# Performance work log

Hardware: AMD Instinct MI355X
Metric: run time of the kernel (lower is better)

The kernel has to match this reference:

```python
import jax, jax.numpy as jnp
import numpy as np

B, H, I, E, K = 512, 1024, 1024, 32, 4
EPS, ALPHA, LIMIT = 1e-5, 1.702, 7.0


def _swiglu(h):
    # interleaved split: even cols -> glu path, odd cols -> linear path
    x_glu = jnp.minimum(h[..., ::2], LIMIT)
    x_lin = jnp.clip(h[..., 1::2], -LIMIT, LIMIT)
    return x_glu * jax.nn.sigmoid(ALPHA * x_glu) * (x_lin + 1.0)


def setup_inputs() -> dict:
    key = jax.random.key(0)
    ks = jax.random.split(key, 7)
    n = lambda k, shape, s: jax.random.normal(k, shape, dtype=jnp.float32) * s
    return {
        "x": n(ks[0], (B, H), 1.0),
        "norm_scale": jnp.ones((H,), jnp.float32),
        "gate_w": n(ks[1], (E, H), 0.02),
        "gate_b": n(ks[2], (E,), 0.02),
        "mlp1_w": n(ks[3], (E, 2 * I, H), 0.02),
        "mlp1_b": n(ks[4], (E, 2 * I), 0.02),
        "mlp2_w": n(ks[5], (E, H, I), 0.02),
        "mlp2_b": n(ks[6], (E, H), 0.02),
    }


def reference(x, norm_scale, gate_w, gate_b, mlp1_w, mlp1_b, mlp2_w, mlp2_b):
    # RMSNorm in fp32
    t = x * jax.lax.rsqrt(jnp.mean(x * x, axis=-1, keepdims=True) + EPS) * norm_scale
    # gate + top-k routing; softmax over the k selected logits
    g = t @ gate_w.T + gate_b                      # [B, E]
    vals, idx = jax.lax.top_k(g, K)                # [B, K]
    w = jax.nn.softmax(vals, axis=-1)              # [B, K]
    # dense routing weights [B, E]: w_dense[b, e] = sum_k w[b,k] * (idx[b,k]==e)
    w_dense = jnp.zeros((t.shape[0], gate_w.shape[0]), t.dtype)
    w_dense = w_dense.at[jnp.arange(t.shape[0])[:, None], idx].add(w)
    # grouped-dense equivalent of the per-token gathered einsum:
    # original: einsum('beck,bk->bec', mlp1_w[idx], t); here we compute all
    # experts densely and combine with w_dense (zero for unselected experts),
    # which is the same math without materializing [B,K,2I,H] weights.
    h = jnp.einsum('bk,eck->bec', t, mlp1_w) + mlp1_b   # [B, E, 2I]
    a = _swiglu(h)                                       # [B, E, I]
    o = jnp.einsum('bei,ehi->beh', a, mlp2_w) + mlp2_b   # [B, E, H]
    y = jnp.einsum('beh,be->bh', o, w_dense)             # [B, H]
    return x + y
```

## Files before the change

### kernel.cpp

```cpp
#include <hip/hip_runtime.h>
#include <hip/hip_bf16.h>
#include <math.h>


#define NB   512
#define NH   1024
#define NI   1024
#define NE   32
#define NK   4
#define N2I  2048
#define CAP  512
#define PADK 40

static constexpr float EPS   = 1e-5f;
static constexpr float ALPHA = 1.702f;
static constexpr float LIMIT = 7.0f;

typedef short bf16x8 __attribute__((ext_vector_type(8)));
typedef float f32x4  __attribute__((ext_vector_type(4)));

__device__ __forceinline__ short hi16(float x) {
    return (short)(__float_as_uint(x) >> 16);
}
__device__ __forceinline__ short lo16(float x) {
    unsigned hb = __float_as_uint(x) & 0xFFFF0000u;
    float r = x - __uint_as_float(hb);
    return (short)(__float_as_uint(r) >> 16);
}
__device__ __forceinline__ void cvt8r(float4 v0, float4 v1,
                                      bf16x8& hh, bf16x8& ll) {
    float f[8] = {v0.x, v0.y, v0.z, v0.w, v1.x, v1.y, v1.z, v1.w};
#pragma unroll
    for (int i = 0; i < 8; i++) { hh[i] = hi16(f[i]); ll[i] = lo16(f[i]); }
}

__global__ __launch_bounds__(256) void k_rms_gate(
    const float* __restrict__ x, const float* __restrict__ scale,
    const float* __restrict__ gw, const float* __restrict__ gb,
    float* __restrict__ t, int* __restrict__ cnt,
    int* __restrict__ tok, int* __restrict__ tke, float* __restrict__ tkw) {
    __shared__ float sh_t[NH];
    __shared__ float sh_red[4];
    __shared__ float sh_g[NE];
    const int b = blockIdx.x, tid = threadIdx.x;
    const int lane = tid & 63, wid = tid >> 6;

    float4 xv = reinterpret_cast<const float4*>(x + (size_t)b * NH)[tid];
    float ss = xv.x * xv.x + xv.y * xv.y + xv.z * xv.z + xv.w * xv.w;
#pragma unroll
    for (int o = 32; o >= 1; o >>= 1) ss += __shfl_down(ss, o);
    if (lane == 0) sh_red[wid] = ss;
    __syncthreads();
    const float tot = sh_red[0] + sh_red[1] + sh_red[2] + sh_red[3];
    const float r = rsqrtf(tot * (1.0f / NH) + EPS);
    float4 sv = reinterpret_cast<const float4*>(scale)[tid];
    float4 tv;
    tv.x = xv.x * r * sv.x; tv.y = xv.y * r * sv.y;
    tv.z = xv.z * r * sv.z; tv.w = xv.w * r * sv.w;
    reinterpret_cast<float4*>(sh_t)[tid] = tv;
    reinterpret_cast<float4*>(t + (size_t)b * NH)[tid] = tv;
    __syncthreads();

#pragma unroll
    for (int q = 0; q < 8; q++) {
        const int e = wid * 8 + q;
        const float* __restrict__ w = gw + (size_t)e * NH;
        float p = 0.f;
#pragma unroll
        for (int i = 0; i < 16; i++) { int k = lane + 64 * i; p += sh_t[k] * w[k]; }
#pragma unroll
        for (int o = 32; o >= 1; o >>= 1) p += __shfl_down(p, o);
        if (lane == 0) sh_g[e] = p + gb[e];
    }
    __syncthreads();

    if (tid == 0) {
        float gv[NE];
#pragma unroll
        for (int e = 0; e < NE; e++) gv[e] = sh_g[e];
        float vals[NK]; int ids[NK];
#pragma unroll
        for (int k = 0; k < NK; k++) {
            int bi = 0; float bv = gv[0];
            for (int e = 1; e < NE; e++) if (gv[e] > bv) { bv = gv[e]; bi = e; }
            vals[k] = bv; ids[k] = bi; gv[bi] = -1e30f;
        }
        const float m = vals[0];
        float s = 0.f, wv[NK];
#pragma unroll
        for (int k = 0; k < NK; k++) { wv[k] = __expf(vals[k] - m); s += wv[k]; }
        const float inv = 1.f / s;
#pragma unroll
        for (int k = 0; k < NK; k++) {
            const int e = ids[k];
            const int pos = atomicAdd(&cnt[e], 1);
            tok[e * CAP + pos] = b;
            tke[b * NK + k] = (e << 16) | pos;
            tkw[b * NK + k] = wv[k] * inv;
        }
    }
}

__global__ void k_prefix(const int* __restrict__ cnt, int* __restrict__ base) {
    if (threadIdx.x == 0) {
        int r = 0;
        for (int e = 0; e < NE; e++) { base[e] = r; r += cnt[e]; }
    }
}

__global__ __launch_bounds__(512, 2) void k_mlp1(
    const float* __restrict__ t, const float* __restrict__ w1,
    const float* __restrict__ b1, const int* __restrict__ cnt,
    const int* __restrict__ base, const int* __restrict__ tok,
    float* __restrict__ a) {
    const int e  = blockIdx.z;
    const int ne = cnt[e];
    const int m0 = blockIdx.y * 128;
    if (m0 >= ne) return;
    const int c0 = blockIdx.x * 128;
    const float* __restrict__ W = w1 + (size_t)e * N2I * NH + (size_t)c0 * NH;

    __shared__ short Ah[128][PADK], Al[128][PADK];
    __shared__ short Bh[128][PADK], Bl[128][PADK];
    __shared__ int   toks[128];

    const int tid = threadIdx.x;
    if (tid < 128) toks[tid] = (m0 + tid < ne) ? tok[e * CAP + m0 + tid] : -1;
    __syncthreads();

    const int lane = tid & 63;
    const int wid  = tid >> 6;
    const int wr = wid >> 1, wc = wid & 1;
    const int frow = lane & 15;
    const int fk   = (lane >> 4) * 8;
    const int srow = tid >> 2;
    const int sc8  = (tid & 3) * 8;

    f32x4 acc[2][4] = {};

    const int tka = toks[srow];
    const float* __restrict__ asrc = t + (size_t)(tka < 0 ? 0 : tka) * NH + sc8;
    const float* __restrict__ bsrc = W + (size_t)srow * NH + sc8;

    float4 ra0 = *(const float4*)(asrc);
    float4 ra1 = *(const float4*)(asrc + 4);
    float4 rb0 = *(const float4*)(bsrc);
    float4 rb1 = *(const float4*)(bsrc + 4);

    for (int k0 = 0; k0 < NH; k0 += 32) {
        bf16x8 hh, ll;
        cvt8r(ra0, ra1, hh, ll);
        if (tka < 0) { hh = (bf16x8)(short)0; ll = (bf16x8)(short)0; }
        *(bf16x8*)&Ah[srow][sc8] = hh;
        *(bf16x8*)&Al[srow][sc8] = ll;
        cvt8r(rb0, rb1, hh, ll);
        *(bf16x8*)&Bh[srow][sc8] = hh;
        *(bf16x8*)&Bl[srow][sc8] = ll;
        if (k0 + 32 < NH) {
            ra0 = *(const float4*)(asrc + k0 + 32);
            ra1 = *(const float4*)(asrc + k0 + 36);
            rb0 = *(const float4*)(bsrc + k0 + 32);
            rb1 = *(const float4*)(bsrc + k0 + 36);
        }
        __syncthreads();

        bf16x8 ah[2], al[2], bh[4], bl[4];
#pragma unroll
        for (int m = 0; m < 2; m++) {
            const int r = wr * 32 + m * 16 + frow;
            ah[m] = *(const bf16x8*)&Ah[r][fk];
            al[m] = *(const bf16x8*)&Al[r][fk];
        }
#pragma unroll
        for (int n = 0; n < 4; n++) {
            const int c = wc * 64 + n * 16 + frow;
            bh[n] = *(const bf16x8*)&Bh[c][fk];
            bl[n] = *(const bf16x8*)&Bl[c][fk];
        }
#pragma unroll
        for (int m = 0; m < 2; m++)
#pragma unroll
            for (int n = 0; n < 4; n++) {
                acc[m][n] = __builtin_amdgcn_mfma_f32_16x16x32_bf16(ah[m], bh[n], acc[m][n], 0, 0, 0);
                acc[m][n] = __builtin_amdgcn_mfma_f32_16x16x32_bf16(ah[m], bl[n], acc[m][n], 0, 0, 0);
                acc[m][n] = __builtin_amdgcn_mfma_f32_16x16x32_bf16(al[m], bh[n], acc[m][n], 0, 0, 0);
            }
        __syncthreads();
    }

    const int slot0 = base[e];
#pragma unroll
    for (int m = 0; m < 2; m++)
#pragma unroll
        for (int n = 0; n < 4; n++) {
            const int gcol = c0 + wc * 64 + n * 16 + frow;
            const float bias = b1[e * N2I + gcol];
            f32x4 v = acc[m][n];
#pragma unroll
            for (int j = 0; j < 4; j++) {
                const float h  = v[j] + bias;
                const float hp = __shfl_xor(h, 1);
                const int row = m0 + wr * 32 + m * 16 + (lane >> 4) * 4 + j;
                if (!(lane & 1) && row < ne) {
                    const float xg = fminf(h, LIMIT);
                    const float xl = fminf(fmaxf(hp, -LIMIT), LIMIT);
                    const float sg2 = 1.f / (1.f + __expf(-ALPHA * xg));
                    a[(size_t)(slot0 + row) * NI + (gcol >> 1)] = xg * sg2 * (xl + 1.f);
                }
            }
        }
}

__global__ __launch_bounds__(512, 2) void k_mlp2(
    const float* __restrict__ a, const float* __restrict__ w2,
    const float* __restrict__ b2, const int* __restrict__ cnt,
    const int* __restrict__ base, float* __restrict__ o) {
    const int e  = blockIdx.z;
    const int ne = cnt[e];
    const int m0 = blockIdx.y * 128;
    if (m0 >= ne) return;
    const int c0 = blockIdx.x * 128;
    const int slot0 = base[e];
    const float* __restrict__ W = w2 + (size_t)e * NH * NI + (size_t)c0 * NI;

    __shared__ short Ah[128][PADK], Al[128][PADK];
    __shared__ short Bh[128][PADK], Bl[128][PADK];

    const int tid = threadIdx.x;
    const int lane = tid & 63;
    const int wid  = tid >> 6;
    const int wr = wid >> 1, wc = wid & 1;
    const int frow = lane & 15;
    const int fk   = (lane >> 4) * 8;
    const int srow = tid >> 2;
    const int sc8  = (tid & 3) * 8;

    f32x4 acc[2][4] = {};

    const int mval = (m0 + srow < ne);
    const float* __restrict__ asrc =
        a + (size_t)(mval ? (slot0 + m0 + srow) : 0) * NI + sc8;
    const float* __restrict__ bsrc = W + (size_t)srow * NI + sc8;

    float4 ra0 = *(const float4*)(asrc);
    float4 ra1 = *(const float4*)(asrc + 4);
    float4 rb0 = *(const float4*)(bsrc);
    float4 rb1 = *(const float4*)(bsrc + 4);

    for (int k0 = 0; k0 < NI; k0 += 32) {
        bf16x8 hh, ll;
        cvt8r(ra0, ra1, hh, ll);
        if (!mval) { hh = (bf16x8)(short)0; ll = (bf16x8)(short)0; }
        *(bf16x8*)&Ah[srow][sc8] = hh;
        *(bf16x8*)&Al[srow][sc8] = ll;
        cvt8r(rb0, rb1, hh, ll);
        *(bf16x8*)&Bh[srow][sc8] = hh;
        *(bf16x8*)&Bl[srow][sc8] = ll;
        if (k0 + 32 < NI) {
            ra0 = *(const float4*)(asrc + k0 + 32);
            ra1 = *(const float4*)(asrc + k0 + 36);
            rb0 = *(const float4*)(bsrc + k0 + 32);
            rb1 = *(const float4*)(bsrc + k0 + 36);
        }
        __syncthreads();

        bf16x8 ah[2], al[2], bh[4], bl[4];
#pragma unroll
        for (int m = 0; m < 2; m++) {
            const int r = wr * 32 + m * 16 + frow;
            ah[m] = *(const bf16x8*)&Ah[r][fk];
            al[m] = *(const bf16x8*)&Al[r][fk];
        }
#pragma unroll
        for (int n = 0; n < 4; n++) {
            const int c = wc * 64 + n * 16 + frow;
            bh[n] = *(const bf16x8*)&Bh[c][fk];
            bl[n] = *(const bf16x8*)&Bl[c][fk];
        }
#pragma unroll
        for (int m = 0; m < 2; m++)
#pragma unroll
            for (int n = 0; n < 4; n++) {
                acc[m][n] = __builtin_amdgcn_mfma_f32_16x16x32_bf16(ah[m], bh[n], acc[m][n], 0, 0, 0);
                acc[m][n] = __builtin_amdgcn_mfma_f32_16x16x32_bf16(ah[m], bl[n], acc[m][n], 0, 0, 0);
                acc[m][n] = __builtin_amdgcn_mfma_f32_16x16x32_bf16(al[m], bh[n], acc[m][n], 0, 0, 0);
            }
        __syncthreads();
    }

#pragma unroll
    for (int m = 0; m < 2; m++)
#pragma unroll
        for (int n = 0; n < 4; n++) {
            const int gcol = c0 + wc * 64 + n * 16 + frow;
            const float bias = b2[e * NH + gcol];
            f32x4 v = acc[m][n];
#pragma unroll
            for (int j = 0; j < 4; j++) {
                const int row = m0 + wr * 32 + m * 16 + (lane >> 4) * 4 + j;
                if (row < ne)
                    o[(size_t)(slot0 + row) * NH + gcol] = v[j] + bias;
            }
        }
}

__global__ __launch_bounds__(256) void k_combine(
    const float* __restrict__ x, const float* __restrict__ o,
    const int* __restrict__ base, const int* __restrict__ tke,
    const float* __restrict__ tkw, float* __restrict__ out) {
    const int b = blockIdx.x, tid = threadIdx.x;
    int slots[NK]; float wk[NK];
#pragma unroll
    for (int k = 0; k < NK; k++) {
        const int v = tke[b * NK + k];
        slots[k] = base[v >> 16] + (v & 0xFFFF);
        wk[k] = tkw[b * NK + k];
    }
    float4 r = reinterpret_cast<const float4*>(x + (size_t)b * NH)[tid];
#pragma unroll
    for (int k = 0; k < NK; k++) {
        float4 ov = reinterpret_cast<const float4*>(o + (size_t)slots[k] * NH)[tid];
        r.x += wk[k] * ov.x; r.y += wk[k] * ov.y;
        r.z += wk[k] * ov.z; r.w += wk[k] * ov.w;
    }
    reinterpret_cast<float4*>(out + (size_t)b * NH)[tid] = r;
}

extern "C" void kernel_launch(void* const* d_in, const int* in_sizes, int n_in,
                              void* d_out, int out_size, void* d_ws, size_t ws_size,
                              hipStream_t stream) {
    const float* x     = (const float*)d_in[0];
    const float* scale = (const float*)d_in[1];
    const float* gw    = (const float*)d_in[2];
    const float* gb    = (const float*)d_in[3];
    const float* w1    = (const float*)d_in[4];
    const float* b1    = (const float*)d_in[5];
    const float* w2    = (const float*)d_in[6];
    const float* b2    = (const float*)d_in[7];
    float* out = (float*)d_out;

    float* t   = (float*)d_ws;
    float* a   = t + (size_t)NB * NH;
    float* o   = a + (size_t)NB * NK * NI;
    int*   tok = (int*)(o + (size_t)NB * NK * NH);
    int*   tke = tok + NE * CAP;
    float* tkw = (float*)(tke + NB * NK);
    int*   cnt = (int*)(tkw + NB * NK);
    int*   bse = cnt + NE;

    hipMemsetAsync(cnt, 0, NE * sizeof(int), stream);
    k_rms_gate<<<NB, 256, 0, stream>>>(x, scale, gw, gb, t, cnt, tok, tke, tkw);
    k_prefix<<<1, 64, 0, stream>>>(cnt, bse);
    k_mlp1<<<dim3(N2I / 128, NB / 128, NE), 512, 0, stream>>>(t, w1, b1, cnt, bse, tok, a);
    k_mlp2<<<dim3(NH / 128, NB / 128, NE), 512, 0, stream>>>(a, w2, b2, cnt, bse, o);
    k_combine<<<NB, 256, 0, stream>>>(x, o, bse, tke, tkw, out);
}
```

Before: 598.6 us.

## Drop weight low-part split, use 4 waves with larger per-wave tiles and double-buffered loads

Weights are now rounded to a single bf16 (round-to-nearest-even) rather than split into hi/lo parts. That removes one of the three MFMAs per tile and the Bl shared buffer, leaving activations as the only operand kept in split precision. Both MLP kernels move from 512 to 256 threads, so each wave computes a 64x64 tile (4x4 accumulators) instead of 32x64, which raises register reuse. Global loads are now double-buffered two K-steps ahead. The price is lower accuracy, because the weight low bits are gone, plus higher register pressure.

```diff
diff --git a/kernel.cpp b/kernel.cpp
--- a/kernel.cpp
+++ b/kernel.cpp
@@ -27,11 +27,20 @@
     float r = x - __uint_as_float(hb);
     return (short)(__float_as_uint(r) >> 16);
 }
-__device__ __forceinline__ void cvt8r(float4 v0, float4 v1,
-                                      bf16x8& hh, bf16x8& ll) {
+__device__ __forceinline__ short rne16(float x) {
+    unsigned u = __float_as_uint(x);
+    return (short)((u + 0x7FFFu + ((u >> 16) & 1u)) >> 16);
+}
+__device__ __forceinline__ void cvtsplit8(float4 v0, float4 v1,
+                                          bf16x8& hh, bf16x8& ll) {
     float f[8] = {v0.x, v0.y, v0.z, v0.w, v1.x, v1.y, v1.z, v1.w};
 #pragma unroll
     for (int i = 0; i < 8; i++) { hh[i] = hi16(f[i]); ll[i] = lo16(f[i]); }
+}
+__device__ __forceinline__ void cvtrne8(float4 v0, float4 v1, bf16x8& hh) {
+    float f[8] = {v0.x, v0.y, v0.z, v0.w, v1.x, v1.y, v1.z, v1.w};
+#pragma unroll
+    for (int i = 0; i < 8; i++) hh[i] = rne16(f[i]);
 }
 
 __global__ __launch_bounds__(256) void k_rms_gate(
@@ -108,7 +117,51 @@
     }
 }
 
-__global__ __launch_bounds__(512, 2) void k_mlp1(
+#define LOADBUF(Aa, Ab, Ac, Ad, Ba, Bb, Bc, Bd, k)                           \
+    do {                                                                     \
+        Aa = *(const float4*)(asrc + (k));      Ab = *(const float4*)(asrc + (k) + 4);  \
+        Ac = *(const float4*)(asrc + (k) + 16); Ad = *(const float4*)(asrc + (k) + 20); \
+        Ba = *(const float4*)(bsrc + (k));      Bb = *(const float4*)(bsrc + (k) + 4);  \
+        Bc = *(const float4*)(bsrc + (k) + 16); Bd = *(const float4*)(bsrc + (k) + 20); \
+    } while (0)
+
+#define CVT_STORE(Aa, Ab, Ac, Ad, Ba, Bb, Bc, Bd)                            \
+    do {                                                                     \
+        bf16x8 hh, ll;                                                       \
+        cvtsplit8(Aa, Ab, hh, ll);                                           \
+        if (zA) { hh = (bf16x8)(short)0; ll = (bf16x8)(short)0; }            \
+        *(bf16x8*)&Ah[srow][sh8] = hh;  *(bf16x8*)&Al[srow][sh8] = ll;       \
+        cvtsplit8(Ac, Ad, hh, ll);                                           \
+        if (zA) { hh = (bf16x8)(short)0; ll = (bf16x8)(short)0; }            \
+        *(bf16x8*)&Ah[srow][sh8 + 16] = hh; *(bf16x8*)&Al[srow][sh8 + 16] = ll; \
+        cvtrne8(Ba, Bb, hh);  *(bf16x8*)&Bh[srow][sh8] = hh;                 \
+        cvtrne8(Bc, Bd, hh);  *(bf16x8*)&Bh[srow][sh8 + 16] = hh;            \
+    } while (0)
+
+#define MFMA_PHASE()                                                         \
+    do {                                                                     \
+        bf16x8 ah[4], al[4], bh[4];                                          \
+        _Pragma("unroll")                                                    \
+        for (int m = 0; m < 4; m++) {                                        \
+            const int r = wr * 64 + m * 16 + frow;                           \
+            ah[m] = *(const bf16x8*)&Ah[r][fk];                              \
+            al[m] = *(const bf16x8*)&Al[r][fk];                              \
+        }                                                                    \
+        _Pragma("unroll")                                                    \
+        for (int n = 0; n < 4; n++) {                                        \
+            const int c = wc * 64 + n * 16 + frow;                           \
+            bh[n] = *(const bf16x8*)&Bh[c][fk];                              \
+        }                                                                    \
+        _Pragma("unroll")                                                    \
+        for (int m = 0; m < 4; m++)                                          \
+            _Pragma("unroll")                                                \
+            for (int n = 0; n < 4; n++) {                                    \
+                acc[m][n] = __builtin_amdgcn_mfma_f32_16x16x32_bf16(ah[m], bh[n], acc[m][n], 0, 0, 0); \
+                acc[m][n] = __builtin_amdgcn_mfma_f32_16x16x32_bf16(al[m], bh[n], acc[m][n], 0, 0, 0); \
+            }                                                                \
+    } while (0)
+
+__global__ __launch_bounds__(256, 2) void k_mlp1(
     const float* __restrict__ t, const float* __restrict__ w1,
     const float* __restrict__ b1, const int* __restrict__ cnt,
     const int* __restrict__ base, const int* __restrict__ tok,
@@ -120,8 +173,7 @@
     const int c0 = blockIdx.x * 128;
     const float* __restrict__ W = w1 + (size_t)e * N2I * NH + (size_t)c0 * NH;
 
-    __shared__ short Ah[128][PADK], Al[128][PADK];
-    __shared__ short Bh[128][PADK], Bl[128][PADK];
+    __shared__ short Ah[128][PADK], Al[128][PADK], Bh[128][PADK];
     __shared__ int   toks[128];
 
     const int tid = threadIdx.x;
@@ -133,64 +185,39 @@
     const int wr = wid >> 1, wc = wid & 1;
     const int frow = lane & 15;
     const int fk   = (lane >> 4) * 8;
-    const int srow = tid >> 2;
-    const int sc8  = (tid & 3) * 8;
-
-    f32x4 acc[2][4] = {};
+    const int srow = tid >> 1;
+    const int sh8  = (tid & 1) * 8;
+
+    f32x4 acc[4][4] = {};
 
     const int tka = toks[srow];
-    const float* __restrict__ asrc = t + (size_t)(tka < 0 ? 0 : tka) * NH + sc8;
-    const float* __restrict__ bsrc = W + (size_t)srow * NH + sc8;
-
-    float4 ra0 = *(const float4*)(asrc);
-    float4 ra1 = *(const float4*)(asrc + 4);
-    float4 rb0 = *(const float4*)(bsrc);
-    float4 rb1 = *(const float4*)(bsrc + 4);
-
-    for (int k0 = 0; k0 < NH; k0 += 32) {
-        bf16x8 hh, ll;
-        cvt8r(ra0, ra1, hh, ll);
-        if (tka < 0) { hh = (bf16x8)(short)0; ll = (bf16x8)(short)0; }
-        *(bf16x8*)&Ah[srow][sc8] = hh;
-        *(bf16x8*)&Al[srow][sc8] = ll;
-        cvt8r(rb0, rb1, hh, ll);
-        *(bf16x8*)&Bh[srow][sc8] = hh;
-        *(bf16x8*)&Bl[srow][sc8] = ll;
-        if (k0 + 32 < NH) {
-            ra0 = *(const float4*)(asrc + k0 + 32);
-            ra1 = *(const float4*)(asrc + k0 + 36);
-            rb0 = *(const float4*)(bsrc + k0 + 32);
-            rb1 = *(const float4*)(bsrc + k0 + 36);
-        }
-        __syncthreads();
-
-        bf16x8 ah[2], al[2], bh[4], bl[4];
-#pragma unroll
-        for (int m = 0; m < 2; m++) {
-            const int r = wr * 32 + m * 16 + frow;
-            ah[m] = *(const bf16x8*)&Ah[r][fk];
-            al[m] = *(const bf16x8*)&Al[r][fk];
-        }
-#pragma unroll
-        for (int n = 0; n < 4; n++) {
-            const int c = wc * 64 + n * 16 + frow;
-            bh[n] = *(const bf16x8*)&Bh[c][fk];
-            bl[n] = *(const bf16x8*)&Bl[c][fk];
-        }
-#pragma unroll
-        for (int m = 0; m < 2; m++)
-#pragma unroll
-            for (int n = 0; n < 4; n++) {
-                acc[m][n] = __builtin_amdgcn_mfma_f32_16x16x32_bf16(ah[m], bh[n], acc[m][n], 0, 0, 0);
-                acc[m][n] = __builtin_amdgcn_mfma_f32_16x16x32_bf16(ah[m], bl[n], acc[m][n], 0, 0, 0);
-                acc[m][n] = __builtin_amdgcn_mfma_f32_16x16x32_bf16(al[m], bh[n], acc[m][n], 0, 0, 0);
-            }
+    const bool zA = (tka < 0);
+    const float* __restrict__ asrc = t + (size_t)(zA ? 0 : tka) * NH + sh8;
+    const float* __restrict__ bsrc = W + (size_t)srow * NH + sh8;
+
+    float4 A0a, A0b, A0c, A0d, B0a, B0b, B0c, B0d;
+    float4 A1a, A1b, A1c, A1d, B1a, B1b, B1c, B1d;
+    LOADBUF(A0a, A0b, A0c, A0d, B0a, B0b, B0c, B0d, 0);
+    LOADBUF(A1a, A1b, A1c, A1d, B1a, B1b, B1c, B1d, 32);
+
+    for (int k0 = 0; k0 < NH; k0 += 64) {
+        CVT_STORE(A0a, A0b, A0c, A0d, B0a, B0b, B0c, B0d);
+        if (k0 + 64 < NH)
+            LOADBUF(A0a, A0b, A0c, A0d, B0a, B0b, B0c, B0d, k0 + 64);
+        __syncthreads();
+        MFMA_PHASE();
+        __syncthreads();
+        CVT_STORE(A1a, A1b, A1c, A1d, B1a, B1b, B1c, B1d);
+        if (k0 + 96 < NH)
+            LOADBUF(A1a, A1b, A1c, A1d, B1a, B1b, B1c, B1d, k0 + 96);
+        __syncthreads();
+        MFMA_PHASE();
         __syncthreads();
     }
 
     const int slot0 = base[e];
 #pragma unroll
-    for (int m = 0; m < 2; m++)
+    for (int m = 0; m < 4; m++)
 #pragma unroll
         for (int n = 0; n < 4; n++) {
             const int gcol = c0 + wc * 64 + n * 16 + frow;
@@ -200,7 +227,7 @@
             for (int j = 0; j < 4; j++) {
                 const float h  = v[j] + bias;
                 const float hp = __shfl_xor(h, 1);
-                const int row = m0 + wr * 32 + m * 16 + (lane >> 4) * 4 + j;
+                const int row = m0 + wr * 64 + m * 16 + (lane >> 4) * 4 + j;
                 if (!(lane & 1) && row < ne) {
                     const float xg = fminf(h, LIMIT);
                     const float xl = fminf(fmaxf(hp, -LIMIT), LIMIT);
@@ -211,7 +238,7 @@
         }
 }
 
-__global__ __launch_bounds__(512, 2) void k_mlp2(
+__global__ __launch_bounds__(256, 2) void k_mlp2(
     const float* __restrict__ a, const float* __restrict__ w2,
     const float* __restrict__ b2, const int* __restrict__ cnt,
     const int* __restrict__ base, float* __restrict__ o) {
@@ -223,8 +250,7 @@
     const int slot0 = base[e];
     const float* __restrict__ W = w2 + (size_t)e * NH * NI + (size_t)c0 * NI;
 
-    __shared__ short Ah[128][PADK], Al[128][PADK];
-    __shared__ short Bh[128][PADK], Bl[128][PADK];
+    __shared__ short Ah[128][PADK], Al[128][PADK], Bh[128][PADK];
 
     const int tid = threadIdx.x;
     const int lane = tid & 63;
@@ -232,64 +258,38 @@
     const int wr = wid >> 1, wc = wid & 1;
     const int frow = lane & 15;
     const int fk   = (lane >> 4) * 8;
-    const int srow = tid >> 2;
-    const int sc8  = (tid & 3) * 8;
-
-    f32x4 acc[2][4] = {};
-
-    const int mval = (m0 + srow < ne);
+    const int srow = tid >> 1;
+    const int sh8  = (tid & 1) * 8;
+
+    f32x4 acc[4][4] = {};
+
+    const bool zA = (m0 + srow >= ne);
     const float* __restrict__ asrc =
-        a + (size_t)(mval ? (slot0 + m0 + srow) : 0) * NI + sc8;
-    const float* __restrict__ bsrc = W + (size_t)srow * NI + sc8;
-
-    float4 ra0 = *(const float4*)(asrc);
-    float4 ra1 = *(const float4*)(asrc + 4);
-    float4 rb0 = *(const float4*)(bsrc);
-    float4 rb1 = *(const float4*)(bsrc + 4);
-
-    for (int k0 = 0; k0 < NI; k0 += 32) {
-        bf16x8 hh, ll;
-        cvt8r(ra0, ra1, hh, ll);
-        if (!mval) { hh = (bf16x8)(short)0; ll = (bf16x8)(short)0; }
-        *(bf16x8*)&Ah[srow][sc8] = hh;
-        *(bf16x8*)&Al[srow][sc8] = ll;
-        cvt8r(rb0, rb1, hh, ll);
-        *(bf16x8*)&Bh[srow][sc8] = hh;
-        *(bf16x8*)&Bl[srow][sc8] = ll;
-        if (k0 + 32 < NI) {
-            ra0 = *(const float4*)(asrc + k0 + 32);
-            ra1 = *(const float4*)(asrc + k0 + 36);
-            rb0 = *(const float4*)(bsrc + k0 + 32);
-            rb1 = *(const float4*)(bsrc + k0 + 36);
-        }
-        __syncthreads();
-
-        bf16x8 ah[2], al[2], bh[4], bl[4];
-#pragma unroll
-        for (int m = 0; m < 2; m++) {
-            const int r = wr * 32 + m * 16 + frow;
-            ah[m] = *(const bf16x8*)&Ah[r][fk];
-            al[m] = *(const bf16x8*)&Al[r][fk];
-        }
-#pragma unroll
-        for (int n = 0; n < 4; n++) {
-            const int c = wc * 64 + n * 16 + frow;
-            bh[n] = *(const bf16x8*)&Bh[c][fk];
-            bl[n] = *(const bf16x8*)&Bl[c][fk];
-        }
-#pragma unroll
-        for (int m = 0; m < 2; m++)
-#pragma unroll
-            for (int n = 0; n < 4; n++) {
-                acc[m][n] = __builtin_amdgcn_mfma_f32_16x16x32_bf16(ah[m], bh[n], acc[m][n], 0, 0, 0);
-                acc[m][n] = __builtin_amdgcn_mfma_f32_16x16x32_bf16(ah[m], bl[n], acc[m][n], 0, 0, 0);
-                acc[m][n] = __builtin_amdgcn_mfma_f32_16x16x32_bf16(al[m], bh[n], acc[m][n], 0, 0, 0);
-            }
-        __syncthreads();
-    }
-
-#pragma unroll
-    for (int m = 0; m < 2; m++)
+        a + (size_t)(zA ? 0 : (slot0 + m0 + srow)) * NI + sh8;
+    const float* __restrict__ bsrc = W + (size_t)srow * NI + sh8;
+
+    float4 A0a, A0b, A0c, A0d, B0a, B0b, B0c, B0d;
+    float4 A1a, A1b, A1c, A1d, B1a, B1b, B1c, B1d;
+    LOADBUF(A0a, A0b, A0c, A0d, B0a, B0b, B0c, B0d, 0);
+    LOADBUF(A1a, A1b, A1c, A1d, B1a, B1b, B1c, B1d, 32);
+
+    for (int k0 = 0; k0 < NI; k0 += 64) {
+        CVT_STORE(A0a, A0b, A0c, A0d, B0a, B0b, B0c, B0d);
+        if (k0 + 64 < NI)
+            LOADBUF(A0a, A0b, A0c, A0d, B0a, B0b, B0c, B0d, k0 + 64);
+        __syncthreads();
+        MFMA_PHASE();
+        __syncthreads();
+        CVT_STORE(A1a, A1b, A1c, A1d, B1a, B1b, B1c, B1d);
+        if (k0 + 96 < NI)
+            LOADBUF(A1a, A1b, A1c, A1d, B1a, B1b, B1c, B1d, k0 + 96);
+        __syncthreads();
+        MFMA_PHASE();
+        __syncthreads();
+    }
+
+#pragma unroll
+    for (int m = 0; m < 4; m++)
 #pragma unroll
         for (int n = 0; n < 4; n++) {
             const int gcol = c0 + wc * 64 + n * 16 + frow;
@@ -297,7 +297,7 @@
             f32x4 v = acc[m][n];
 #pragma unroll
             for (int j = 0; j < 4; j++) {
-                const int row = m0 + wr * 32 + m * 16 + (lane >> 4) * 4 + j;
+                const int row = m0 + wr * 64 + m * 16 + (lane >> 4) * 4 + j;
                 if (row < ne)
                     o[(size_t)(slot0 + row) * NH + gcol] = v[j] + bias;
             }
@@ -351,7 +351,7 @@
     hipMemsetAsync(cnt, 0, NE * sizeof(int), stream);
     k_rms_gate<<<NB, 256, 0, stream>>>(x, scale, gw, gb, t, cnt, tok, tke, tkw);
     k_prefix<<<1, 64, 0, stream>>>(cnt, bse);
-    k_mlp1<<<dim3(N2I / 128, NB / 128, NE), 512, 0, stream>>>(t, w1, b1, cnt, bse, tok, a);
-    k_mlp2<<<dim3(NH / 128, NB / 128, NE), 512, 0, stream>>>(a, w2, b2, cnt, bse, o);
+    k_mlp1<<<dim3(N2I / 128, NB / 128, NE), 256, 0, stream>>>(t, w1, b1, cnt, bse, tok, a);
+    k_mlp2<<<dim3(NH / 128, NB / 128, NE), 256, 0, stream>>>(a, w2, b2, cnt, bse, o);
     k_combine<<<NB, 256, 0, stream>>>(x, o, bse, tke, tkw, out);
 }
```

Measured after the change: 594.0 us. No clear change (-0.8%).
